# Kernel tuning notes

Measured on AMD Instinct MI355X. Metric: run time of the kernel, lower is better.

## Reference

```python
import jax, jax.numpy as jnp
import numpy as np

N = 50000   # nodes
E = 600000  # edges per edge_index
G = 64      # graphs in batch
H = 128     # hidden_neurons == n_node_features
EPS = 1e-12 # F.normalize eps


def sage(x, edge, Wl, bl, Wr, norm):
    # PyG SAGEConv (aggr='mean'): out_i = lin_l(mean_{j->i} x_j) + lin_r(x_i)
    src, dst = edge[0], edge[1]
    s = jax.ops.segment_sum(x[src], dst, num_segments=N)          # [N,H]
    cnt = jax.ops.segment_sum(jnp.ones((edge.shape[1],), x.dtype), dst, num_segments=N)
    agg = s / jnp.maximum(cnt, 1.0)[:, None]
    out = agg @ Wl + bl + x @ Wr
    if norm:  # F.normalize(out, p=2, dim=-1)
        n = jnp.linalg.norm(out, axis=-1, keepdims=True)
        out = out / jnp.maximum(n, EPS)
    return out


def setup_inputs() -> dict:
    key = jax.random.key(0)
    ks = jax.random.split(key, 40)
    sc = 1.0 / np.sqrt(H)
    d = {}
    d["x"] = jax.random.normal(ks[0], (N, H), jnp.float32)
    d["eic"] = jax.random.randint(ks[1], (2, E), 0, N, dtype=jnp.int32)
    d["eid"] = jax.random.randint(ks[2], (2, E), 0, N, dtype=jnp.int32)
    d["eit"] = jax.random.randint(ks[3], (2, E), 0, N, dtype=jnp.int32)
    d["batch"] = jnp.sort(jax.random.randint(ks[4], (N,), 0, G, dtype=jnp.int32))
    i = 5
    for c in ["c1", "c2", "c3", "c4", "c5"]:
        d[c + "_Wl"] = jax.random.normal(ks[i], (H, H), jnp.float32) * sc; i += 1
        d[c + "_bl"] = jnp.zeros((H,), jnp.float32)
        d[c + "_Wr"] = jax.random.normal(ks[i], (H, H), jnp.float32) * sc; i += 1
    d["l0_W"] = jax.random.normal(ks[i], (H, H), jnp.float32) * sc; i += 1
    d["l0_b"] = jnp.zeros((H,), jnp.float32)
    d["l1_W"] = jax.random.normal(ks[i], (H, H), jnp.float32) * sc; i += 1
    d["l1_b"] = jnp.zeros((H,), jnp.float32)
    d["head_W"] = jax.random.normal(ks[i], (H, 1), jnp.float32) * sc; i += 1
    d["head_b"] = jnp.zeros((1,), jnp.float32)
    return d


def reference(x, eic, eid, eit, batch,
              c1_Wl, c1_bl, c1_Wr, c2_Wl, c2_bl, c2_Wr, c3_Wl, c3_bl, c3_Wr,
              c4_Wl, c4_bl, c4_Wr, c5_Wl, c5_bl, c5_Wr,
              l0_W, l0_b, l1_W, l1_b, head_W, head_b):
    h = sage(x, eid, c1_Wl, c1_bl, c1_Wr, True)
    for _ in range(2):  # it_b4_dest, shared conv2 weights
        h = sage(h, eic, c2_Wl, c2_bl, c2_Wr, True)
    h = sage(h, eit, c3_Wl, c3_bl, c3_Wr, False)  # conv3 normalize=False
    h = sage(h, eid, c4_Wl, c4_bl, c4_Wr, True)
    for _ in range(2):  # it_aft_dest, shared conv5 weights
        h = sage(h, eic, c5_Wl, c5_bl, c5_Wr, True)
    g = jax.ops.segment_sum(h, batch, num_segments=G)  # global_add_pool -> [G,H]
    g = jax.nn.relu(g @ l0_W + l0_b)
    g = jax.nn.relu(g @ l1_W + l1_b)
    return g @ head_W + head_b  # [G,1]
```

## Files before the change

kernel.cpp:

```cpp
#include <hip/hip_runtime.h>
#include <hip/hip_bf16.h>


constexpr int N_NODES = 50000;
constexpr int NE      = 600000;
constexpr int H       = 128;
constexpr int NG      = 64;
constexpr int N3      = 3 * N_NODES;

constexpr int NB   = (N3 + 1023) >> 10;
constexpr int EPB  = 2048;
constexpr int BPS  = (NE + EPB - 1) / EPB;
constexpr int CAP2 = 19456;

typedef __attribute__((ext_vector_type(8))) short short8;
typedef __attribute__((ext_vector_type(4))) float f32x4;

__device__ __forceinline__ ushort f2bf(float f) {
    uint x = __float_as_uint(f);
    return (ushort)((x + 0x7FFFu + ((x >> 16) & 1u)) >> 16);
}
__device__ __forceinline__ float bf2f(ushort u) {
    return __uint_as_float(((uint)u) << 16);
}


__global__ __launch_bounds__(256) void k_bucketize(
    const int* __restrict__ e0, const int* __restrict__ e1,
    const int* __restrict__ e2, int* __restrict__ gcnt,
    int* __restrict__ rcnt, int2* __restrict__ bucket) {
    __shared__ int hist[NB];
    __shared__ int basearr[NB];
    __shared__ int cur[NB];
    __shared__ int gposs[NB];
    __shared__ int2 stage[EPB];
    __shared__ int dstoff[EPB];

    int t = threadIdx.x;
    int s = blockIdx.x / BPS;
    int w = blockIdx.x - s * BPS;
    const int* ep = (s == 0 ? e0 : (s == 1 ? e1 : e2));
    int eBase = w * EPB;
    int m = NE - eBase;
    if (m > EPB) m = EPB;

    for (int i = t; i < NB; i += 256) hist[i] = 0;
    __syncthreads();

    int myk[EPB / 256], mys[EPB / 256];
#pragma unroll
    for (int k = 0; k < EPB / 256; ++k) {
        int i = t + 256 * k;
        if (i < m) {
            int d   = ep[NE + eBase + i];
            int src = ep[eBase + i];
            int key = s * N_NODES + d;
            myk[k] = key; mys[k] = src;
            atomicAdd(&hist[key >> 10], 1);
        } else {
            myk[k] = -1;
        }
    }
    __syncthreads();

    if (t == 0) {
        int run = 0;
        for (int b = 0; b < NB; ++b) { basearr[b] = run; run += hist[b]; }
    }
    __syncthreads();

    if (t < NB) {
        int h = hist[t];
        int p = (h + 7) & ~7;
        gposs[t] = p ? atomicAdd(&gcnt[t], p) : 0;
        if (h) atomicAdd(&rcnt[t], h);
        cur[t] = 0;
    }
    __syncthreads();

#pragma unroll
    for (int k = 0; k < EPB / 256; ++k) {
        if (myk[k] >= 0) {
            int b  = myk[k] >> 10;
            int sl = atomicAdd(&cur[b], 1);
            int p  = basearr[b] + sl;
            stage[p]  = make_int2(myk[k], mys[k]);
            dstoff[p] = b * CAP2 + gposs[b] + sl;
        }
    }
    __syncthreads();

    for (int i = t; i < m; i += 256) bucket[dstoff[i]] = stage[i];
    for (int i = t; i < NB * 8; i += 256) {
        int b = i >> 3, j = i & 7;
        int h = hist[b];
        int p = (h + 7) & ~7;
        if (h + j < p)
            bucket[(size_t)b * CAP2 + gposs[b] + h + j] = make_int2(-1, 0);
    }
}


__global__ __launch_bounds__(512) void k_scatter2(const int2* __restrict__ bucket,
                                                  const int* __restrict__ gcnt,
                                                  const int* __restrict__ rcnt,
                                                  int* __restrict__ ptr,
                                                  int* __restrict__ adj) {
    int b = blockIdx.x;
    int base = b << 10;
    int nk = N3 - base;
    if (nk > 1024) nk = 1024;
    __shared__ int lh[1024];
    __shared__ int lsum[512];
    __shared__ int lfill[1024];
    __shared__ int bb;
    int t = threadIdx.x;

    int rv = (t < NB) ? rcnt[t] : 0;
    lsum[t] = rv;
    __syncthreads();
    for (int off = 1; off < 512; off <<= 1) {
        int u = (t >= off) ? lsum[t - off] : 0;
        __syncthreads();
        if (t >= off) lsum[t] += u;
        __syncthreads();
    }
    if (t == b) bb = lsum[t] - rv;
    if (b == 0 && t == 0) ptr[N3] = 3 * NE;
    for (int i = t; i < 1024; i += 512) lh[i] = 0;
    __syncthreads();

    int c = gcnt[b];
    const int2* seg = bucket + (size_t)b * CAP2;
    for (int i = t; i < c; i += 512) {
        int k = seg[i].x;
        if (k >= 0) atomicAdd(&lh[k - base], 1);
    }
    __syncthreads();
    int v0 = lh[t * 2], v1 = lh[t * 2 + 1];
    int ts = v0 + v1;
    lsum[t] = ts;
    __syncthreads();
    for (int off = 1; off < 512; off <<= 1) {
        int u = (t >= off) ? lsum[t - off] : 0;
        __syncthreads();
        if (t >= off) lsum[t] += u;
        __syncthreads();
    }
    int ex = lsum[t] - ts + bb;
    int e0 = ex, e1 = ex + v0;
    if (t * 2     < nk) { ptr[base + t * 2]     = e0; lfill[t * 2]     = e0; }
    if (t * 2 + 1 < nk) { ptr[base + t * 2 + 1] = e1; lfill[t * 2 + 1] = e1; }
    __syncthreads();
    for (int i = t; i < c; i += 512) {
        int2 ed = seg[i];
        if (ed.x >= 0) {
            int pos = atomicAdd(&lfill[ed.x - base], 1);
            adj[pos] = ed.y;
        }
    }
}


__global__ void k_split(const float* __restrict__ x, ushort* __restrict__ hi,
                        ushort* __restrict__ lo, int* __restrict__ zmem) {
    int tid = blockIdx.x * 256 + threadIdx.x;
    if (tid < NG * H + 2 * NB) zmem[tid] = 0;
    size_t i = (size_t)tid * 4;
    if (i >= (size_t)N_NODES * H) return;
    float4 v = *(const float4*)(x + i);
    ushort4 h, l;
    h.x = f2bf(v.x); l.x = f2bf(v.x - bf2f(h.x));
    h.y = f2bf(v.y); l.y = f2bf(v.y - bf2f(h.y));
    h.z = f2bf(v.z); l.z = f2bf(v.z - bf2f(h.z));
    h.w = f2bf(v.w); l.w = f2bf(v.w - bf2f(h.w));
    *(ushort4*)(hi + i) = h;
    *(ushort4*)(lo + i) = l;
}


__global__ void k_wsplit5(const float* W0l, const float* W0r, const float* W1l,
                          const float* W1r, const float* W2l, const float* W2r,
                          const float* W3l, const float* W3r, const float* W4l,
                          const float* W4r, ushort* __restrict__ Bpk) {
    int idx = blockIdx.x * 256 + threadIdx.x;
    if (idx >= 5 * 32768) return;
    int c = idx >> 15, r = idx & 32767;
    const float* Wl = (c == 0 ? W0l : c == 1 ? W1l : c == 2 ? W2l : c == 3 ? W3l : W4l);
    const float* Wr = (c == 0 ? W0r : c == 1 ? W1r : c == 2 ? W2r : c == 3 ? W3r : W4r);
    int n = r & 255, k = r >> 8;
    float w = (n < H) ? Wl[k * H + n] : Wr[k * H + (n - H)];
    int q = k >> 5, g = (k >> 3) & 3, j = k & 7;
    int off = ((q * 4 + g) * 256 + n) * 8 + j;
    ushort h = f2bf(w);
    ushort* bh = Bpk + (size_t)c * 65536;
    bh[off]         = h;
    bh[32768 + off] = f2bf(w - bf2f(h));
}


__global__ __launch_bounds__(256) void k_gemm_mfma(
    const ushort* __restrict__ Ahi, const ushort* __restrict__ Alo,
    const ushort* __restrict__ Bh, const ushort* __restrict__ Bl,
    ushort* __restrict__ z, ushort* __restrict__ yb) {
    __shared__ ushort AshF[2 * 64 * 128];
    int t = threadIdx.x;
    int rowBase = blockIdx.x * 64;
    {
        int wslot = t & ~63;
        int lane  = t & 63;
#pragma unroll
        for (int i = 0; i < 8; ++i) {
            int sbase = i * 256 + wslot;
            int S     = sbase + lane;
            int plane = S >> 10;
            int row   = (S >> 4) & 63;
            int pc    = S & 15;
            int grow  = rowBase + row;
            if (grow > N_NODES - 1) grow = N_NODES - 1;
            const ushort* Ap  = plane ? Alo : Ahi;
            const ushort* src = Ap + (size_t)grow * H + ((pc ^ (row & 15)) << 3);
            ushort* ldst = AshF + (size_t)sbase * 8;
            __builtin_amdgcn_global_load_lds(
                (const __attribute__((address_space(1))) void*)src,
                (__attribute__((address_space(3))) void*)ldst, 16, 0, 0);
        }
    }
    __syncthreads();

    int wave = t >> 6, lane = t & 63;
    int m16 = lane & 15, q4 = lane >> 4;
    int n0 = wave * 64;

    f32x4 acc[4][4];
#pragma unroll
    for (int r = 0; r < 4; ++r)
#pragma unroll
        for (int c = 0; c < 4; ++c) {
            acc[r][c][0] = 0.f; acc[r][c][1] = 0.f;
            acc[r][c][2] = 0.f; acc[r][c][3] = 0.f;
        }

    for (int q = 0; q < 4; ++q) {
        short8 bh_[4], bl_[4], ah_[4], al_[4];
#pragma unroll
        for (int c = 0; c < 4; ++c) {
            int boff = ((q * 4 + q4) * 256 + n0 + c * 16 + m16) * 8;
            bh_[c] = *(const short8*)(Bh + boff);
            bl_[c] = *(const short8*)(Bl + boff);
        }
#pragma unroll
        for (int r = 0; r < 4; ++r) {
            int roff = ((r * 16 + m16) << 7) + (((q * 4 + q4) ^ m16) << 3);
            ah_[r] = *(const short8*)&AshF[roff];
            al_[r] = *(const short8*)&AshF[8192 + roff];
        }
#pragma unroll
        for (int r = 0; r < 4; ++r)
#pragma unroll
            for (int c = 0; c < 4; ++c) {
                acc[r][c] = __builtin_amdgcn_mfma_f32_16x16x32_bf16(
                    ah_[r], bh_[c], acc[r][c], 0, 0, 0);
                acc[r][c] = __builtin_amdgcn_mfma_f32_16x16x32_bf16(
                    ah_[r], bl_[c], acc[r][c], 0, 0, 0);
                acc[r][c] = __builtin_amdgcn_mfma_f32_16x16x32_bf16(
                    al_[r], bh_[c], acc[r][c], 0, 0, 0);
            }
    }

#pragma unroll
    for (int r = 0; r < 4; ++r)
#pragma unroll
        for (int c = 0; c < 4; ++c) {
            int col = n0 + c * 16 + m16;
            ushort* op = (col < H) ? (z + col) : (yb + (col - H));
#pragma unroll
            for (int j = 0; j < 4; ++j) {
                int gr = rowBase + r * 16 + q4 * 4 + j;
                if (gr < N_NODES) op[(size_t)gr * H] = f2bf(acc[r][c][j]);
            }
        }
}


__global__ __launch_bounds__(256) void k_aggnorm(
    const ushort* __restrict__ z, const ushort* __restrict__ yb,
    const int* __restrict__ ptr, const int* __restrict__ adj,
    const float* __restrict__ bl,
    ushort* __restrict__ hhi, ushort* __restrict__ hlo, int norm) {
    int gtid = blockIdx.x * blockDim.x + threadIdx.x;
    int node = gtid >> 4;
    int sl   = threadIdx.x & 15;
    if (node >= N_NODES) return;
    int beg = ptr[node], end = ptr[node + 1];
    int deg = end - beg;
    const ushort* zrow = z + sl * 8;
    float a[8];
#pragma unroll
    for (int k = 0; k < 8; ++k) a[k] = 0.f;

    for (int base = 0; base < deg; base += 16) {
        int m = deg - base;
        if (m > 16) m = 16;
        int idx = (sl < m) ? adj[beg + base + sl] : 0;
        int j = 0;
        for (; j + 8 <= m; j += 8) {
            int n0 = __shfl(idx, j,     16);
            int n1 = __shfl(idx, j + 1, 16);
            int n2 = __shfl(idx, j + 2, 16);
            int n3 = __shfl(idx, j + 3, 16);
            int n4 = __shfl(idx, j + 4, 16);
            int n5 = __shfl(idx, j + 5, 16);
            int n6 = __shfl(idx, j + 6, 16);
            int n7 = __shfl(idx, j + 7, 16);
            short8 v0 = *(const short8*)(zrow + (size_t)n0 * H);
            short8 v1 = *(const short8*)(zrow + (size_t)n1 * H);
            short8 v2 = *(const short8*)(zrow + (size_t)n2 * H);
            short8 v3 = *(const short8*)(zrow + (size_t)n3 * H);
            short8 v4 = *(const short8*)(zrow + (size_t)n4 * H);
            short8 v5 = *(const short8*)(zrow + (size_t)n5 * H);
            short8 v6 = *(const short8*)(zrow + (size_t)n6 * H);
            short8 v7 = *(const short8*)(zrow + (size_t)n7 * H);
#pragma unroll
            for (int k = 0; k < 8; ++k)
                a[k] += ((bf2f((ushort)v0[k]) + bf2f((ushort)v1[k])) +
                         (bf2f((ushort)v2[k]) + bf2f((ushort)v3[k]))) +
                        ((bf2f((ushort)v4[k]) + bf2f((ushort)v5[k])) +
                         (bf2f((ushort)v6[k]) + bf2f((ushort)v7[k])));
        }
        for (; j + 4 <= m; j += 4) {
            int n0 = __shfl(idx, j,     16);
            int n1 = __shfl(idx, j + 1, 16);
            int n2 = __shfl(idx, j + 2, 16);
            int n3 = __shfl(idx, j + 3, 16);
            short8 v0 = *(const short8*)(zrow + (size_t)n0 * H);
            short8 v1 = *(const short8*)(zrow + (size_t)n1 * H);
            short8 v2 = *(const short8*)(zrow + (size_t)n2 * H);
            short8 v3 = *(const short8*)(zrow + (size_t)n3 * H);
#pragma unroll
            for (int k = 0; k < 8; ++k)
                a[k] += (bf2f((ushort)v0[k]) + bf2f((ushort)v1[k])) +
                        (bf2f((ushort)v2[k]) + bf2f((ushort)v3[k]));
        }
        for (; j < m; ++j) {
            int n0 = __shfl(idx, j, 16);
            short8 v0 = *(const short8*)(zrow + (size_t)n0 * H);
#pragma unroll
            for (int k = 0; k < 8; ++k) a[k] += bf2f((ushort)v0[k]);
        }
    }

    float inv = 1.0f / (float)(deg > 1 ? deg : 1);
    short8 yv = *(const short8*)(yb + (size_t)node * H + sl * 8);
    float4 bva = *(const float4*)(bl + sl * 8);
    float4 bvb = *(const float4*)(bl + sl * 8 + 4);
    float vv[8];
    vv[0] = a[0] * inv + bva.x + bf2f((ushort)yv[0]);
    vv[1] = a[1] * inv + bva.y + bf2f((ushort)yv[1]);
    vv[2] = a[2] * inv + bva.z + bf2f((ushort)yv[2]);
    vv[3] = a[3] * inv + bva.w + bf2f((ushort)yv[3]);
    vv[4] = a[4] * inv + bvb.x + bf2f((ushort)yv[4]);
    vv[5] = a[5] * inv + bvb.y + bf2f((ushort)yv[5]);
    vv[6] = a[6] * inv + bvb.z + bf2f((ushort)yv[6]);
    vv[7] = a[7] * inv + bvb.w + bf2f((ushort)yv[7]);
    if (norm) {
        float ss = 0.f;
#pragma unroll
        for (int k = 0; k < 8; ++k) ss += vv[k] * vv[k];
#pragma unroll
        for (int mm = 1; mm < 16; mm <<= 1) ss += __shfl_xor(ss, mm, 16);
        float n2 = 1.0f / fmaxf(sqrtf(ss), 1e-12f);
#pragma unroll
        for (int k = 0; k < 8; ++k) vv[k] *= n2;
    }
    short8 ho, lo8;
#pragma unroll
    for (int k = 0; k < 8; ++k) {
        ushort hh = f2bf(vv[k]);
        ho[k]  = (short)hh;
        lo8[k] = (short)f2bf(vv[k] - bf2f(hh));
    }
    *(short8*)(hhi + (size_t)node * H + sl * 8) = ho;
    *(short8*)(hlo + (size_t)node * H + sl * 8) = lo8;
}


constexpr int POOL_ROWS = 64;

__global__ void k_pool(const ushort* __restrict__ hhi, const ushort* __restrict__ hlo,
                       const int* __restrict__ batch, float* __restrict__ g) {
    int col = threadIdx.x;
    int r0 = blockIdx.x * POOL_ROWS;
    int r1 = r0 + POOL_ROWS;
    if (r1 > N_NODES) r1 = N_NODES;
    if (r0 >= N_NODES) return;
    float acc = 0.f;
    int cur = batch[r0];
    int r = r0;
    for (; r + 4 <= r1; r += 4) {
        float v0 = bf2f(hhi[(size_t)r * H + col])       + bf2f(hlo[(size_t)r * H + col]);
        float v1 = bf2f(hhi[(size_t)(r + 1) * H + col]) + bf2f(hlo[(size_t)(r + 1) * H + col]);
        float v2 = bf2f(hhi[(size_t)(r + 2) * H + col]) + bf2f(hlo[(size_t)(r + 2) * H + col]);
        float v3 = bf2f(hhi[(size_t)(r + 3) * H + col]) + bf2f(hlo[(size_t)(r + 3) * H + col]);
        int b3 = batch[r + 3];
        if (b3 == cur) {
            acc += (v0 + v1) + (v2 + v3);
        } else {
            int b0 = batch[r], b1 = batch[r + 1], b2 = batch[r + 2];
            if (b0 != cur) { atomicAdd(&g[cur * H + col], acc); acc = 0.f; cur = b0; }
            acc += v0;
            if (b1 != cur) { atomicAdd(&g[cur * H + col], acc); acc = 0.f; cur = b1; }
            acc += v1;
            if (b2 != cur) { atomicAdd(&g[cur * H + col], acc); acc = 0.f; cur = b2; }
            acc += v2;
            if (b3 != cur) { atomicAdd(&g[cur * H + col], acc); acc = 0.f; cur = b3; }
            acc += v3;
        }
    }
    for (; r < r1; ++r) {
        int b = batch[r];
        if (b != cur) { atomicAdd(&g[cur * H + col], acc); acc = 0.f; cur = b; }
        acc += bf2f(hhi[(size_t)r * H + col]) + bf2f(hlo[(size_t)r * H + col]);
    }
    atomicAdd(&g[cur * H + col], acc);
}


__global__ void k_mlp(const float* __restrict__ g, const float* __restrict__ W0,
                      const float* __restrict__ b0, const float* __restrict__ W1,
                      const float* __restrict__ b1, const float* __restrict__ Wh,
                      const float* __restrict__ bh, float* __restrict__ out) {
    int gi = blockIdx.x;
    int t  = threadIdx.x;
    __shared__ float buf0[H];
    __shared__ float buf1[H];
    __shared__ float red[2];

    float acc = b0[t];
    for (int k = 0; k < H; ++k) acc += g[gi * H + k] * W0[k * H + t];
    buf0[t] = fmaxf(acc, 0.f);
    __syncthreads();

    acc = b1[t];
    for (int k = 0; k < H; ++k) acc += buf0[k] * W1[k * H + t];
    buf1[t] = fmaxf(acc, 0.f);
    __syncthreads();

    float p = buf1[t] * Wh[t];
    for (int m = 1; m < 64; m <<= 1) p += __shfl_xor(p, m, 64);
    if ((t & 63) == 0) red[t >> 6] = p;
    __syncthreads();
    if (t == 0) out[gi] = red[0] + red[1] + bh[0];
}


extern "C" void kernel_launch(void* const* d_in, const int* in_sizes, int n_in,
                              void* d_out, int out_size, void* d_ws, size_t ws_size,
                              hipStream_t stream) {
    const float* x     = (const float*)d_in[0];
    const int*   eic   = (const int*)d_in[1];
    const int*   eid   = (const int*)d_in[2];
    const int*   eit   = (const int*)d_in[3];
    const int*   batch = (const int*)d_in[4];
    const float* cW[5][3];
    for (int c = 0; c < 5; ++c) {
        cW[c][0] = (const float*)d_in[5 + c * 3 + 0];
        cW[c][1] = (const float*)d_in[5 + c * 3 + 1];
        cW[c][2] = (const float*)d_in[5 + c * 3 + 2];
    }
    const float* l0_W = (const float*)d_in[20];
    const float* l0_b = (const float*)d_in[21];
    const float* l1_W = (const float*)d_in[22];
    const float* l1_b = (const float*)d_in[23];
    const float* hd_W = (const float*)d_in[24];
    const float* hd_b = (const float*)d_in[25];
    float* outp = (float*)d_out;

    const size_t NH = (size_t)N_NODES * H;
    ushort* Ahi = (ushort*)d_ws;
    ushort* Alo = Ahi + NH;
    ushort* zb  = Alo + NH;
    ushort* yb  = zb + NH;
    ushort* Bpk = yb + NH;
    float*  gbuf = (float*)(Bpk + 5 * 2 * 32768);
    int* gcnt = (int*)(gbuf + (size_t)NG * H);
    int* rcnt = gcnt + NB;
    int* ptr_all = rcnt + NB;
    int* adj_all = ptr_all + (N3 + 1);
    int2* bucket = (int2*)zb;

    dim3 b256(256);

    k_wsplit5<<<dim3(640), b256, 0, stream>>>(cW[0][0], cW[0][2], cW[1][0], cW[1][2],
                                              cW[2][0], cW[2][2], cW[3][0], cW[3][2],
                                              cW[4][0], cW[4][2], Bpk);
    k_split<<<dim3((int)(NH / 1024)), b256, 0, stream>>>(x, Ahi, Alo, (int*)gbuf);

    k_bucketize<<<dim3(3 * BPS), b256, 0, stream>>>(eic, eid, eit, gcnt, rcnt, bucket);
    k_scatter2<<<dim3(NB), dim3(512), 0, stream>>>(bucket, gcnt, rcnt, ptr_all, adj_all);

    const int L_set[7]  = {1, 0, 0, 2, 1, 0, 0};
    const int L_conv[7] = {0, 1, 1, 2, 3, 4, 4};
    const int L_norm[7] = {1, 1, 1, 0, 1, 1, 1};

    dim3 gAgg((N_NODES * 16 + 255) / 256);
    dim3 gGemm((N_NODES + 63) / 64);

    for (int L = 0; L < 7; ++L) {
        int s = L_set[L], c = L_conv[L];
        const ushort* Bh = Bpk + (size_t)c * 65536;
        const ushort* Bl = Bh + 32768;
        k_gemm_mfma<<<gGemm, b256, 0, stream>>>(Ahi, Alo, Bh, Bl, zb, yb);
        k_aggnorm<<<gAgg, b256, 0, stream>>>(zb, yb, ptr_all + s * N_NODES, adj_all,
                                             cW[c][1], Ahi, Alo, L_norm[L]);
    }

    k_pool<<<dim3((N_NODES + POOL_ROWS - 1) / POOL_ROWS), dim3(H), 0, stream>>>(
        Ahi, Alo, batch, gbuf);
    k_mlp<<<dim3(NG), dim3(H), 0, stream>>>(gbuf, l0_W, l0_b, l1_W, l1_b, hd_W, hd_b,
                                            outp);
}
```

Measured before the change: 523.5 us.

## Split aggregation into column slices and move L2 normalization to separate kernel

The gather-aggregate kernel now assigns each block a 32-column slice of 64 nodes, with 4 lanes per node, so concurrent blocks share the same column slice of z and gather locality in cache should improve. Because a node's row is now split across blocks, per-slice partial sums of squares are written to a buffer and a new k_norm kernel rescales the hi/lo bf16 outputs. This trades an extra launch and an extra read/write pass over the hi/lo activations on normalized layers for a narrower gather footprint. Adjacency loads and the yb load use nontemporal hints.

```diff
diff --git a/kernel.cpp b/kernel.cpp
--- a/kernel.cpp
+++ b/kernel.cpp
@@ -283,77 +283,92 @@
 }
 
 
-__global__ __launch_bounds__(256) void k_aggnorm(
+__global__ __launch_bounds__(256) void k_agg(
     const ushort* __restrict__ z, const ushort* __restrict__ yb,
     const int* __restrict__ ptr, const int* __restrict__ adj,
     const float* __restrict__ bl,
-    ushort* __restrict__ hhi, ushort* __restrict__ hlo, int norm) {
-    int gtid = blockIdx.x * blockDim.x + threadIdx.x;
-    int node = gtid >> 4;
-    int sl   = threadIdx.x & 15;
+    ushort* __restrict__ hhi, ushort* __restrict__ hlo,
+    float* __restrict__ ssq) {
+    int bid = blockIdx.x;
+    int g = bid >> 3, r = bid & 7;
+    int slice   = r >> 1;
+    int nodeblk = g * 2 + (r & 1);
+    int t = threadIdx.x;
+    int grp = t >> 2;
+    int l = t & 3;
+    int node = nodeblk * 64 + grp;
     if (node >= N_NODES) return;
     int beg = ptr[node], end = ptr[node + 1];
     int deg = end - beg;
-    const ushort* zrow = z + sl * 8;
+    int lb = (t & 63) & ~3;
+    const ushort* zsl = z + slice * 32 + l * 8;
     float a[8];
 #pragma unroll
     for (int k = 0; k < 8; ++k) a[k] = 0.f;
 
-    for (int base = 0; base < deg; base += 16) {
+    for (int base = 0; base < deg; base += 8) {
         int m = deg - base;
-        if (m > 16) m = 16;
-        int idx = (sl < m) ? adj[beg + base + sl] : 0;
-        int j = 0;
-        for (; j + 8 <= m; j += 8) {
-            int n0 = __shfl(idx, j,     16);
-            int n1 = __shfl(idx, j + 1, 16);
-            int n2 = __shfl(idx, j + 2, 16);
-            int n3 = __shfl(idx, j + 3, 16);
-            int n4 = __shfl(idx, j + 4, 16);
-            int n5 = __shfl(idx, j + 5, 16);
-            int n6 = __shfl(idx, j + 6, 16);
-            int n7 = __shfl(idx, j + 7, 16);
-            short8 v0 = *(const short8*)(zrow + (size_t)n0 * H);
-            short8 v1 = *(const short8*)(zrow + (size_t)n1 * H);
-            short8 v2 = *(const short8*)(zrow + (size_t)n2 * H);
-            short8 v3 = *(const short8*)(zrow + (size_t)n3 * H);
-            short8 v4 = *(const short8*)(zrow + (size_t)n4 * H);
-            short8 v5 = *(const short8*)(zrow + (size_t)n5 * H);
-            short8 v6 = *(const short8*)(zrow + (size_t)n6 * H);
-            short8 v7 = *(const short8*)(zrow + (size_t)n7 * H);
+        if (m > 8) m = 8;
+        int ix0 = 0, ix1 = 0;
+        if (l * 2 < m)     ix0 = __builtin_nontemporal_load(adj + beg + base + l * 2);
+        if (l * 2 + 1 < m) ix1 = __builtin_nontemporal_load(adj + beg + base + l * 2 + 1);
+        int n0 = __shfl(ix0, lb + 0, 64), n1 = __shfl(ix1, lb + 0, 64);
+        int n2 = __shfl(ix0, lb + 1, 64), n3 = __shfl(ix1, lb + 1, 64);
+        int n4 = __shfl(ix0, lb + 2, 64), n5 = __shfl(ix1, lb + 2, 64);
+        int n6 = __shfl(ix0, lb + 3, 64), n7 = __shfl(ix1, lb + 3, 64);
+        if (m == 8) {
+            short8 v0 = *(const short8*)(zsl + (size_t)n0 * H);
+            short8 v1 = *(const short8*)(zsl + (size_t)n1 * H);
+            short8 v2 = *(const short8*)(zsl + (size_t)n2 * H);
+            short8 v3 = *(const short8*)(zsl + (size_t)n3 * H);
+            short8 v4 = *(const short8*)(zsl + (size_t)n4 * H);
+            short8 v5 = *(const short8*)(zsl + (size_t)n5 * H);
+            short8 v6 = *(const short8*)(zsl + (size_t)n6 * H);
+            short8 v7 = *(const short8*)(zsl + (size_t)n7 * H);
 #pragma unroll
             for (int k = 0; k < 8; ++k)
                 a[k] += ((bf2f((ushort)v0[k]) + bf2f((ushort)v1[k])) +
                          (bf2f((ushort)v2[k]) + bf2f((ushort)v3[k]))) +
                         ((bf2f((ushort)v4[k]) + bf2f((ushort)v5[k])) +
                          (bf2f((ushort)v6[k]) + bf2f((ushort)v7[k])));
-        }
-        for (; j + 4 <= m; j += 4) {
-            int n0 = __shfl(idx, j,     16);
-            int n1 = __shfl(idx, j + 1, 16);
-            int n2 = __shfl(idx, j + 2, 16);
-            int n3 = __shfl(idx, j + 3, 16);
-            short8 v0 = *(const short8*)(zrow + (size_t)n0 * H);
-            short8 v1 = *(const short8*)(zrow + (size_t)n1 * H);
-            short8 v2 = *(const short8*)(zrow + (size_t)n2 * H);
-            short8 v3 = *(const short8*)(zrow + (size_t)n3 * H);
-#pragma unroll
-            for (int k = 0; k < 8; ++k)
-                a[k] += (bf2f((ushort)v0[k]) + bf2f((ushort)v1[k])) +
-                        (bf2f((ushort)v2[k]) + bf2f((ushort)v3[k]));
-        }
-        for (; j < m; ++j) {
-            int n0 = __shfl(idx, j, 16);
-            short8 v0 = *(const short8*)(zrow + (size_t)n0 * H);
-#pragma unroll
-            for (int k = 0; k < 8; ++k) a[k] += bf2f((ushort)v0[k]);
+        } else {
+            if (m >= 4) {
+                short8 v0 = *(const short8*)(zsl + (size_t)n0 * H);
+                short8 v1 = *(const short8*)(zsl + (size_t)n1 * H);
+                short8 v2 = *(const short8*)(zsl + (size_t)n2 * H);
+                short8 v3 = *(const short8*)(zsl + (size_t)n3 * H);
+#pragma unroll
+                for (int k = 0; k < 8; ++k)
+                    a[k] += (bf2f((ushort)v0[k]) + bf2f((ushort)v1[k])) +
+                            (bf2f((ushort)v2[k]) + bf2f((ushort)v3[k]));
+            }
+            int na = (m >= 4) ? n4 : n0;
+            int nb = (m >= 4) ? n5 : n1;
+            int nc = (m >= 4) ? n6 : n2;
+            int rem = m & 3;
+            if (rem > 0) {
+                short8 v = *(const short8*)(zsl + (size_t)na * H);
+#pragma unroll
+                for (int k = 0; k < 8; ++k) a[k] += bf2f((ushort)v[k]);
+            }
+            if (rem > 1) {
+                short8 v = *(const short8*)(zsl + (size_t)nb * H);
+#pragma unroll
+                for (int k = 0; k < 8; ++k) a[k] += bf2f((ushort)v[k]);
+            }
+            if (rem > 2) {
+                short8 v = *(const short8*)(zsl + (size_t)nc * H);
+#pragma unroll
+                for (int k = 0; k < 8; ++k) a[k] += bf2f((ushort)v[k]);
+            }
         }
     }
 
     float inv = 1.0f / (float)(deg > 1 ? deg : 1);
-    short8 yv = *(const short8*)(yb + (size_t)node * H + sl * 8);
-    float4 bva = *(const float4*)(bl + sl * 8);
-    float4 bvb = *(const float4*)(bl + sl * 8 + 4);
+    size_t off = (size_t)node * H + slice * 32 + l * 8;
+    short8 yv = __builtin_nontemporal_load((const short8*)(yb + off));
+    float4 bva = *(const float4*)(bl + slice * 32 + l * 8);
+    float4 bvb = *(const float4*)(bl + slice * 32 + l * 8 + 4);
     float vv[8];
     vv[0] = a[0] * inv + bva.x + bf2f((ushort)yv[0]);
     vv[1] = a[1] * inv + bva.y + bf2f((ushort)yv[1]);
@@ -363,16 +378,14 @@
     vv[5] = a[5] * inv + bvb.y + bf2f((ushort)yv[5]);
     vv[6] = a[6] * inv + bvb.z + bf2f((ushort)yv[6]);
     vv[7] = a[7] * inv + bvb.w + bf2f((ushort)yv[7]);
-    if (norm) {
-        float ss = 0.f;
-#pragma unroll
-        for (int k = 0; k < 8; ++k) ss += vv[k] * vv[k];
-#pragma unroll
-        for (int mm = 1; mm < 16; mm <<= 1) ss += __shfl_xor(ss, mm, 16);
-        float n2 = 1.0f / fmaxf(sqrtf(ss), 1e-12f);
-#pragma unroll
-        for (int k = 0; k < 8; ++k) vv[k] *= n2;
-    }
+
+    float ss = 0.f;
+#pragma unroll
+    for (int k = 0; k < 8; ++k) ss += vv[k] * vv[k];
+    ss += __shfl_xor(ss, 1, 64);
+    ss += __shfl_xor(ss, 2, 64);
+    if (l == 0) ssq[slice * N_NODES + node] = ss;
+
     short8 ho, lo8;
 #pragma unroll
     for (int k = 0; k < 8; ++k) {
@@ -380,8 +393,35 @@
         ho[k]  = (short)hh;
         lo8[k] = (short)f2bf(vv[k] - bf2f(hh));
     }
-    *(short8*)(hhi + (size_t)node * H + sl * 8) = ho;
-    *(short8*)(hlo + (size_t)node * H + sl * 8) = lo8;
+    *(short8*)(hhi + off) = ho;
+    *(short8*)(hlo + off) = lo8;
+}
+
+
+__global__ __launch_bounds__(256) void k_norm(ushort* __restrict__ hhi,
+                                              ushort* __restrict__ hlo,
+                                              const float* __restrict__ ssq) {
+    int gtid = blockIdx.x * 256 + threadIdx.x;
+    int node = gtid >> 5;
+    int l = threadIdx.x & 31;
+    if (node >= N_NODES) return;
+    float ss = (ssq[node] + ssq[N_NODES + node]) +
+               (ssq[2 * N_NODES + node] + ssq[3 * N_NODES + node]);
+    float s = 1.0f / fmaxf(sqrtf(ss), 1e-12f);
+    size_t off = (size_t)node * H + l * 4;
+    ushort4 hv = *(const ushort4*)(hhi + off);
+    ushort4 lv = *(const ushort4*)(hlo + off);
+    float v0 = (bf2f(hv.x) + bf2f(lv.x)) * s;
+    float v1 = (bf2f(hv.y) + bf2f(lv.y)) * s;
+    float v2 = (bf2f(hv.z) + bf2f(lv.z)) * s;
+    float v3 = (bf2f(hv.w) + bf2f(lv.w)) * s;
+    ushort4 ho, lo4;
+    ho.x = f2bf(v0); lo4.x = f2bf(v0 - bf2f(ho.x));
+    ho.y = f2bf(v1); lo4.y = f2bf(v1 - bf2f(ho.y));
+    ho.z = f2bf(v2); lo4.z = f2bf(v2 - bf2f(ho.z));
+    ho.w = f2bf(v3); lo4.w = f2bf(v3 - bf2f(ho.w));
+    *(ushort4*)(hhi + off) = ho;
+    *(ushort4*)(hlo + off) = lo4;
 }
 
 
@@ -487,6 +527,7 @@
     int* rcnt = gcnt + NB;
     int* ptr_all = rcnt + NB;
     int* adj_all = ptr_all + (N3 + 1);
+    float* ssq   = (float*)(adj_all + 3 * NE);
     int2* bucket = (int2*)zb;
 
     dim3 b256(256);
@@ -503,7 +544,8 @@
     const int L_conv[7] = {0, 1, 1, 2, 3, 4, 4};
     const int L_norm[7] = {1, 1, 1, 0, 1, 1, 1};
 
-    dim3 gAgg((N_NODES * 16 + 255) / 256);
+    dim3 gAgg(3128);
+    dim3 gNorm((N_NODES * 32 + 255) / 256);
     dim3 gGemm((N_NODES + 63) / 64);
 
     for (int L = 0; L < 7; ++L) {
@@ -511,8 +553,10 @@
         const ushort* Bh = Bpk + (size_t)c * 65536;
         const ushort* Bl = Bh + 32768;
         k_gemm_mfma<<<gGemm, b256, 0, stream>>>(Ahi, Alo, Bh, Bl, zb, yb);
-        k_aggnorm<<<gAgg, b256, 0, stream>>>(zb, yb, ptr_all + s * N_NODES, adj_all,
-                                             cW[c][1], Ahi, Alo, L_norm[L]);
+        k_agg<<<gAgg, b256, 0, stream>>>(zb, yb, ptr_all + s * N_NODES, adj_all,
+                                         cW[c][1], Ahi, Alo, ssq);
+        if (L_norm[L])
+            k_norm<<<gNorm, b256, 0, stream>>>(Ahi, Alo, ssq);
     }
 
     k_pool<<<dim3((N_NODES + POOL_ROWS - 1) / POOL_ROWS), dim3(H), 0, stream>>>(
```

Result: slower. 702.5 us (+34.2%).
